# Kernel optimization log

Measured on AMD Instinct MI355X. Metric: run time of the kernel, lower is better.

## Reference

```python
import jax, jax.numpy as jnp
import numpy as np

B, D, C = 512, 512, 85742   # batch, in_features, out_features (MS1M identities)
M = 4                       # angular margin order -> cos(4*theta) = 8c^4 - 8c^2 + 1
PI = 3.14159265             # constant used in the torch source
LAMB = max(5.0, 1000.0 * (1.0 + 0.12 * 1) ** -1.0)  # lamb at iter=1 (first forward)
EPS = 1e-12                 # torch F.normalize eps


def setup_inputs() -> dict:
    key = jax.random.key(0)
    k1, k2, k3 = jax.random.split(key, 3)
    x = jax.random.normal(k1, (B, D), dtype=jnp.float32)
    label = jax.random.randint(k2, (B,), 0, C)
    limit = np.sqrt(6.0 / (D + C))  # xavier_uniform bound for weight [C, D]
    weight = jax.random.uniform(k3, (C, D), minval=-limit, maxval=limit, dtype=jnp.float32)
    return {"x": x, "weight": weight, "label": label}


def reference(x, weight, label):
    # row-normalize features and class weights (F.normalize, p=2, dim=1)
    xn = x / jnp.maximum(jnp.linalg.norm(x, axis=1, keepdims=True), EPS)
    wn = weight / jnp.maximum(jnp.linalg.norm(weight, axis=1, keepdims=True), EPS)
    cos = jnp.clip(xn @ wn.T, -1.0, 1.0)                       # [B, C] cosine logits
    cos_m = 8.0 * cos**4 - 8.0 * cos**2 + 1.0                  # cos(4*theta), m=4
    # theta/k computed on detached cos (torch uses cos_theta.data)
    theta = jnp.arccos(jax.lax.stop_gradient(cos))
    k = jnp.floor(M * theta / PI)
    phi = (-1.0) ** k * cos_m - 2.0 * k                        # [B, C]
    feat_norm = jnp.linalg.norm(x, axis=1)                     # [B]
    one_hot = jax.nn.one_hot(label, C, dtype=cos.dtype)        # scatter of 1s at label
    out = (one_hot * (phi - cos) / (1.0 + LAMB) + cos) * feat_norm[:, None]
    # cross-entropy, mean reduction
    logp = jax.nn.log_softmax(out, axis=1)
    loss = -jnp.take_along_axis(logp, label[:, None], axis=1).mean()
    return loss
```

## Files before the change

kernel.cpp:

```cpp
#include <hip/hip_runtime.h>
#include <stdint.h>

#define D_K 512
#define C_CLS 85742
#define N_PART 1340

using bf16x8 = __attribute__((ext_vector_type(8))) short;
using f32x4  = __attribute__((ext_vector_type(4))) float;

__device__ __forceinline__ unsigned int cvtpk(float a, float b) {
  unsigned int r;
  asm("v_cvt_pk_bf16_f32 %0, %1, %2" : "=v"(r) : "v"(a), "v"(b));
  return r;
}
__device__ __forceinline__ unsigned short f2bf(float f) {
  unsigned int u = __builtin_bit_cast(unsigned int, f);
  u += 0x7FFFu + ((u >> 16) & 1u);
  return (unsigned short)(u >> 16);
}
__device__ __forceinline__ float bf2f(unsigned short h) {
  return __builtin_bit_cast(float, ((unsigned int)h) << 16);
}
__device__ __forceinline__ float sq8(const float4& a, const float4& b) {
  return a.x*a.x + a.y*a.y + a.z*a.z + a.w*a.w +
         b.x*b.x + b.y*b.y + b.z*b.z + b.w*b.w;
}

#define GLDS(srcp, dstp) __builtin_amdgcn_global_load_lds( \
    (const __attribute__((address_space(1))) unsigned int*)(srcp), \
    (__attribute__((address_space(3))) unsigned int*)(dstp), 16, 0, 0)

__global__ __launch_bounds__(256) void k_xnorm(const float* __restrict__ X,
                                               unsigned short* __restrict__ XN,
                                               float* __restrict__ FN) {
  int row  = blockIdx.x * 4 + (threadIdx.x >> 6);
  int lane = threadIdx.x & 63;
  const float4* px = (const float4*)(X + (size_t)row * D_K + lane * 8);
  float4 u = px[0], v = px[1];
  float nsq = sq8(u, v);
#pragma unroll
  for (int m = 1; m <= 32; m <<= 1) nsq += __shfl_xor(nsq, m);
  float nrm = sqrtf(nsq);
  float inv = 1.0f / fmaxf(nrm, 1e-12f);
  uint4 o;
  o.x = cvtpk(u.x*inv, u.y*inv); o.y = cvtpk(u.z*inv, u.w*inv);
  o.z = cvtpk(v.x*inv, v.y*inv); o.w = cvtpk(v.z*inv, v.w*inv);
  *(uint4*)(XN + (size_t)row * D_K + lane * 8) = o;
  if (lane == 0) FN[row] = nrm;
}

__global__ __launch_bounds__(512, 2) void k_gemm_lse(const float* __restrict__ W,
                                                     const unsigned short* __restrict__ XN,
                                                     const float* __restrict__ FN,
                                                     float2* __restrict__ PART) {
  __shared__ alignas(16) unsigned short As[2][16384];
  __shared__ alignas(16) unsigned short Bs[2][2560];
  __shared__ float nsqS[64];

  int bid = blockIdx.x;
  int xcd = bid & 7, loc = bid >> 3;
  int nb = (xcd < 4 ? xcd * 168 : 4 * 168 + (xcd - 4) * 167) + loc;
  int n0 = nb * 64;

  int t    = threadIdx.x;
  int lane = t & 63, wid = t >> 6;
  int s = lane & 15, g = lane >> 4;

  int rAl = lane >> 2;
  int lcA = (lane & 3) ^ ((lane >> 3) & 3);
  const unsigned short* gA0 = XN + (size_t)(wid * 64 + rAl) * D_K + lcA * 8;
  const unsigned short* gA1 = gA0 + (size_t)16 * D_K;
  const unsigned short* gA2 = gA0 + (size_t)32 * D_K;
  const unsigned short* gA3 = gA0 + (size_t)48 * D_K;

  int rB = t >> 3, c8 = t & 7;
  int grB = n0 + rB; if (grB > C_CLS - 1) grB = C_CLS - 1;
  const float* pB = W + (size_t)grB * D_K + c8 * 4;

  f32x4 acc[4][4] = {};
  float nsq = 0.f;
  float4 bx, by;

#define STAGE_A(b, kk) do { \
    GLDS(gA0 + (size_t)(kk) * 32, &As[b][wid * 2048 +    0]); \
    GLDS(gA1 + (size_t)(kk) * 32, &As[b][wid * 2048 +  512]); \
    GLDS(gA2 + (size_t)(kk) * 32, &As[b][wid * 2048 + 1024]); \
    GLDS(gA3 + (size_t)(kk) * 32, &As[b][wid * 2048 + 1536]); \
  } while (0)

#define LDB4(kk) (*(const float4*)(pB + (size_t)(kk) * 32))

#define CVTW(bv, b) do { \
    nsq += bv.x * bv.x + bv.y * bv.y + bv.z * bv.z + bv.w * bv.w; \
    uint2 u_ = make_uint2(cvtpk(bv.x, bv.y), cvtpk(bv.z, bv.w)); \
    *(uint2*)(&Bs[b][rB * 40 + c8 * 4]) = u_; \
  } while (0)

#define FRAGS_MFMA(b) do { \
    bf16x8 af[4], bfr[4]; \
    _Pragma("unroll") for (int mf = 0; mf < 4; ++mf) \
      af[mf] = *(const bf16x8*)(&As[b][(wid * 64 + mf * 16 + s) * 32 + (g ^ ((s >> 1) & 3)) * 8]); \
    _Pragma("unroll") for (int nf = 0; nf < 4; ++nf) \
      bfr[nf] = *(const bf16x8*)(&Bs[b][(nf * 16 + s) * 40 + g * 8]); \
    _Pragma("unroll") for (int mf = 0; mf < 4; ++mf) \
      _Pragma("unroll") for (int nf = 0; nf < 4; ++nf) \
        acc[mf][nf] = __builtin_amdgcn_mfma_f32_16x16x32_bf16(af[mf], bfr[nf], acc[mf][nf], 0, 0, 0); \
  } while (0)

#define BARC1() do { \
    asm volatile("s_waitcnt vmcnt(1) lgkmcnt(0)" ::: "memory"); \
    __builtin_amdgcn_s_barrier(); } while (0)
#define BAR0() do { \
    asm volatile("s_waitcnt vmcnt(0) lgkmcnt(0)" ::: "memory"); \
    __builtin_amdgcn_s_barrier(); } while (0)

  STAGE_A(0, 0);
  bx = LDB4(0);
  by = LDB4(1);
  CVTW(bx, 0);
  BARC1();

  for (int kt = 0; kt < 14; kt += 2) {
    STAGE_A(1, kt + 1);
    bx = LDB4(kt + 2);
    FRAGS_MFMA(0);
    CVTW(by, 1);
    BARC1();
    STAGE_A(0, kt + 2);
    by = LDB4(kt + 3);
    FRAGS_MFMA(1);
    CVTW(bx, 0);
    BARC1();
  }
  STAGE_A(1, 15);
  FRAGS_MFMA(0);
  CVTW(by, 1);
  BAR0();
  FRAGS_MFMA(1);

  nsq += __shfl_xor(nsq, 1); nsq += __shfl_xor(nsq, 2); nsq += __shfl_xor(nsq, 4);
  if (c8 == 0) nsqS[rB] = nsq;
  __syncthreads();

  float rinv[4]; int cvalid[4];
#pragma unroll
  for (int nf = 0; nf < 4; ++nf) {
    cvalid[nf] = (n0 + nf * 16 + s) < C_CLS;
    rinv[nf] = 1.0f / fmaxf(sqrtf(nsqS[nf * 16 + s]), 1e-12f);
  }
  const float NEG_INF = -__builtin_inff();
#pragma unroll
  for (int mf = 0; mf < 4; ++mf) {
#pragma unroll
    for (int q = 0; q < 4; ++q) {
      int rl = wid * 64 + mf * 16 + g * 4 + q;
      float fr = FN[rl];
      float z[4]; float mx = NEG_INF;
#pragma unroll
      for (int nf = 0; nf < 4; ++nf) {
        float cc = acc[mf][nf][q] * rinv[nf];
        cc = fminf(fmaxf(cc, -1.0f), 1.0f);
        z[nf] = cvalid[nf] ? cc * fr : NEG_INF;
        mx = fmaxf(mx, z[nf]);
      }
#pragma unroll
      for (int d = 1; d <= 8; d <<= 1) mx = fmaxf(mx, __shfl_xor(mx, d));
      float se = 0.f;
#pragma unroll
      for (int nf = 0; nf < 4; ++nf) se += __expf(z[nf] - mx);
#pragma unroll
      for (int d = 1; d <= 8; d <<= 1) se += __shfl_xor(se, d);
      if (s == mf * 4 + q)
        PART[(size_t)rl * N_PART + nb] = make_float2(mx, se);
    }
  }
}

__global__ __launch_bounds__(64) void k_target(const float* __restrict__ W,
                                               const unsigned short* __restrict__ XN,
                                               const float* __restrict__ FN,
                                               const int* __restrict__ LBL,
                                               float2* __restrict__ ZT) {
  int row = blockIdx.x;
  int lane = threadIdx.x;
  int lab = LBL[row];
  const float* pw = W + (size_t)lab * D_K + lane * 8;
  const unsigned short* px = XN + (size_t)row * D_K + lane * 8;
  float dot = 0.f, nsq = 0.f;
#pragma unroll
  for (int j = 0; j < 8; ++j) {
    float w = pw[j];
    nsq += w * w;
    dot += bf2f(px[j]) * bf2f(f2bf(w));
  }
#pragma unroll
  for (int m = 1; m <= 32; m <<= 1) { dot += __shfl_xor(dot, m); nsq += __shfl_xor(nsq, m); }
  if (lane == 0) {
    const float LAMB = 1000.0f / 1.12f;
    float rinv = 1.0f / fmaxf(sqrtf(nsq), 1e-12f);
    float c = fminf(fmaxf(dot * rinv, -1.0f), 1.0f);
    float c2 = c * c;
    float cm = 8.0f * c2 * c2 - 8.0f * c2 + 1.0f;
    float th = acosf(c);
    float kf = floorf(4.0f * th / 3.14159265f);
    float phi = ((((int)kf) & 1) ? -cm : cm) - 2.0f * kf;
    float fr = FN[row];
    float zu = fr * c;
    float zm = fr * (c + (phi - c) / (1.0f + LAMB));
    ZT[row] = make_float2(zu, zm);
  }
}

__global__ __launch_bounds__(256) void k_lse(const float2* __restrict__ PART,
                                             const float2* __restrict__ ZT,
                                             float* __restrict__ LOSSI) {
  int row = blockIdx.x;
  int t = threadIdx.x;
  const float NEG_INF = -__builtin_inff();
  float m = NEG_INF, ss = 0.f;
  for (int p = t; p < N_PART; p += 256) {
    float2 ps = PART[(size_t)row * N_PART + p];
    if (ps.y > 0.f) {
      if (ps.x > m) { ss = ss * __expf(m - ps.x) + ps.y; m = ps.x; }
      else          { ss += ps.y * __expf(ps.x - m); }
    }
  }
  __shared__ float sm[256], sv[256];
  sm[t] = m; sv[t] = ss;
  __syncthreads();
  for (int o = 128; o > 0; o >>= 1) {
    if (t < o) {
      float m1 = sm[t], s1 = sv[t];
      float m2 = sm[t + o], s2 = sv[t + o];
      float mm = fmaxf(m1, m2);
      float e1 = (m1 > NEG_INF) ? s1 * __expf(m1 - mm) : 0.f;
      float e2 = (m2 > NEG_INF) ? s2 * __expf(m2 - mm) : 0.f;
      sm[t] = mm; sv[t] = e1 + e2;
    }
    __syncthreads();
  }
  if (t == 0) {
    float M = sm[0], S = sv[0];
    float2 zt = ZT[row];
    S += __expf(zt.y - M) - __expf(zt.x - M);
    LOSSI[row] = M + logf(S) - zt.y;
  }
}

__global__ __launch_bounds__(256) void k_mean(const float* __restrict__ LOSSI,
                                              float* __restrict__ OUT) {
  int t = threadIdx.x;
  float s_ = LOSSI[t] + LOSSI[t + 256];
#pragma unroll
  for (int m = 1; m <= 32; m <<= 1) s_ += __shfl_xor(s_, m);
  __shared__ float wsum[4];
  if ((t & 63) == 0) wsum[t >> 6] = s_;
  __syncthreads();
  if (t == 0) OUT[0] = (wsum[0] + wsum[1] + wsum[2] + wsum[3]) * (1.0f / 512.0f);
}

extern "C" void kernel_launch(void* const* d_in, const int* in_sizes, int n_in,
                              void* d_out, int out_size, void* d_ws, size_t ws_size,
                              hipStream_t stream) {
  const float* X   = (const float*)d_in[0];
  const float* W   = (const float*)d_in[1];
  const int*   LBL = (const int*)d_in[2];
  float* OUT = (float*)d_out;

  char* ws = (char*)d_ws;
  unsigned short* XN = (unsigned short*)ws;
  float*  FN    = (float*)(ws + 524288);
  float2* ZT    = (float2*)(ws + 526336);
  float*  LOSSI = (float*)(ws + 530432);
  float2* PART  = (float2*)(ws + 532480);

  k_xnorm  <<<dim3(128),  dim3(256), 0, stream>>>(X, XN, FN);
  k_gemm_lse<<<dim3(1340), dim3(512), 0, stream>>>(W, XN, FN, PART);
  k_target <<<dim3(512),  dim3(64),  0, stream>>>(W, XN, FN, LBL, ZT);
  k_lse    <<<dim3(512),  dim3(256), 0, stream>>>(PART, ZT, LOSSI);
  k_mean   <<<dim3(1),    dim3(256), 0, stream>>>(LOSSI, OUT);
}
```

Baseline: 107.9 us.

## Load A fragments directly from global instead of staging through LDS

Removes the global_load_lds staging of the normalized-feature tile (A) into shared memory and instead has each lane read its bf16x8 A fragments straight from global/L2 right before the MFMAs. This cuts LDS footprint and LDS traffic, which could allow more occupancy. It also drops the XCD-aware block remapping in favour of a plain blockIdx mapping. The trade-off is that global loads now sit directly on the MFMA critical path without prefetch, and L2 locality per XCD may change.

```diff
diff --git a/kernel.cpp b/kernel.cpp
--- a/kernel.cpp
+++ b/kernel.cpp
@@ -25,10 +25,6 @@
   return a.x*a.x + a.y*a.y + a.z*a.z + a.w*a.w +
          b.x*b.x + b.y*b.y + b.z*b.z + b.w*b.w;
 }
-
-#define GLDS(srcp, dstp) __builtin_amdgcn_global_load_lds( \
-    (const __attribute__((address_space(1))) unsigned int*)(srcp), \
-    (__attribute__((address_space(3))) unsigned int*)(dstp), 16, 0, 0)
 
 __global__ __launch_bounds__(256) void k_xnorm(const float* __restrict__ X,
                                                unsigned short* __restrict__ XN,
@@ -53,25 +49,20 @@
                                                      const unsigned short* __restrict__ XN,
                                                      const float* __restrict__ FN,
                                                      float2* __restrict__ PART) {
-  __shared__ alignas(16) unsigned short As[2][16384];
-  __shared__ alignas(16) unsigned short Bs[2][2560];
+  __shared__ alignas(16) unsigned short Bs[2][64 * 40];
   __shared__ float nsqS[64];
 
-  int bid = blockIdx.x;
-  int xcd = bid & 7, loc = bid >> 3;
-  int nb = (xcd < 4 ? xcd * 168 : 4 * 168 + (xcd - 4) * 167) + loc;
+  int nb = blockIdx.x;
   int n0 = nb * 64;
 
   int t    = threadIdx.x;
   int lane = t & 63, wid = t >> 6;
   int s = lane & 15, g = lane >> 4;
 
-  int rAl = lane >> 2;
-  int lcA = (lane & 3) ^ ((lane >> 3) & 3);
-  const unsigned short* gA0 = XN + (size_t)(wid * 64 + rAl) * D_K + lcA * 8;
-  const unsigned short* gA1 = gA0 + (size_t)16 * D_K;
-  const unsigned short* gA2 = gA0 + (size_t)32 * D_K;
-  const unsigned short* gA3 = gA0 + (size_t)48 * D_K;
+  const unsigned short* pA0 = XN + (size_t)(wid * 64 + s) * D_K + g * 8;
+  const unsigned short* pA1 = pA0 + (size_t)16 * D_K;
+  const unsigned short* pA2 = pA0 + (size_t)32 * D_K;
+  const unsigned short* pA3 = pA0 + (size_t)48 * D_K;
 
   int rB = t >> 3, c8 = t & 7;
   int grB = n0 + rB; if (grB > C_CLS - 1) grB = C_CLS - 1;
@@ -80,13 +71,6 @@
   f32x4 acc[4][4] = {};
   float nsq = 0.f;
   float4 bx, by;
-
-#define STAGE_A(b, kk) do { \
-    GLDS(gA0 + (size_t)(kk) * 32, &As[b][wid * 2048 +    0]); \
-    GLDS(gA1 + (size_t)(kk) * 32, &As[b][wid * 2048 +  512]); \
-    GLDS(gA2 + (size_t)(kk) * 32, &As[b][wid * 2048 + 1024]); \
-    GLDS(gA3 + (size_t)(kk) * 32, &As[b][wid * 2048 + 1536]); \
-  } while (0)
 
 #define LDB4(kk) (*(const float4*)(pB + (size_t)(kk) * 32))
 
@@ -96,10 +80,12 @@
     *(uint2*)(&Bs[b][rB * 40 + c8 * 4]) = u_; \
   } while (0)
 
-#define FRAGS_MFMA(b) do { \
+#define FRAGS_MFMA(b, kk) do { \
     bf16x8 af[4], bfr[4]; \
-    _Pragma("unroll") for (int mf = 0; mf < 4; ++mf) \
-      af[mf] = *(const bf16x8*)(&As[b][(wid * 64 + mf * 16 + s) * 32 + (g ^ ((s >> 1) & 3)) * 8]); \
+    af[0] = *(const bf16x8*)(pA0 + (size_t)(kk) * 32); \
+    af[1] = *(const bf16x8*)(pA1 + (size_t)(kk) * 32); \
+    af[2] = *(const bf16x8*)(pA2 + (size_t)(kk) * 32); \
+    af[3] = *(const bf16x8*)(pA3 + (size_t)(kk) * 32); \
     _Pragma("unroll") for (int nf = 0; nf < 4; ++nf) \
       bfr[nf] = *(const bf16x8*)(&Bs[b][(nf * 16 + s) * 40 + g * 8]); \
     _Pragma("unroll") for (int mf = 0; mf < 4; ++mf) \
@@ -114,29 +100,25 @@
     asm volatile("s_waitcnt vmcnt(0) lgkmcnt(0)" ::: "memory"); \
     __builtin_amdgcn_s_barrier(); } while (0)
 
-  STAGE_A(0, 0);
   bx = LDB4(0);
   by = LDB4(1);
   CVTW(bx, 0);
   BARC1();
 
   for (int kt = 0; kt < 14; kt += 2) {
-    STAGE_A(1, kt + 1);
     bx = LDB4(kt + 2);
-    FRAGS_MFMA(0);
+    FRAGS_MFMA(0, kt);
     CVTW(by, 1);
     BARC1();
-    STAGE_A(0, kt + 2);
     by = LDB4(kt + 3);
-    FRAGS_MFMA(1);
+    FRAGS_MFMA(1, kt + 1);
     CVTW(bx, 0);
     BARC1();
   }
-  STAGE_A(1, 15);
-  FRAGS_MFMA(0);
+  FRAGS_MFMA(0, 14);
   CVTW(by, 1);
   BAR0();
-  FRAGS_MFMA(1);
+  FRAGS_MFMA(1, 15);
 
   nsq += __shfl_xor(nsq, 1); nsq += __shfl_xor(nsq, 2); nsq += __shfl_xor(nsq, 4);
   if (c8 == 0) nsqS[rB] = nsq;
```

Result: slower. 191.4 us (+77.3%).
